# Performance work log

Hardware: AMD Instinct MI355X
Metric: run time of the kernel (lower is better)

Reference implementation:

```python
import jax, jax.numpy as jnp
import numpy as np

B, M, N, K = 8192, 512, 2048, 16
P = 50      # top-k support size per iteration
EPS = 0.01


def soft_threshold(x, theta, p):
    # x: [B, N]
    if p == 0:
        return jnp.sign(x) * jax.nn.relu(jnp.abs(x) - theta)
    abs_ = jnp.abs(x)
    topk_vals, _ = jax.lax.top_k(abs_, p)          # sorted descending
    thresh = topk_vals[:, -1]                      # min of top-k, per row
    keep = (abs_ > thresh[:, None]).astype(x.dtype)
    shrunk = jnp.sign(x) * jax.nn.relu(abs_ - theta)
    return keep * x + (1.0 - keep) * shrunk


def setup_inputs() -> dict:
    key = jax.random.key(0)
    k_y, k_A = jax.random.split(key)
    y = jax.random.normal(k_y, (B, M), dtype=jnp.float32)
    A = jax.random.normal(k_A, (M, N), dtype=jnp.float32) / np.sqrt(M)
    gamma = jnp.full((K,), 3.0, dtype=jnp.float32)
    theta = jnp.full((K,), 0.02, dtype=jnp.float32)
    a_param = jnp.full((K,), 0.01, dtype=jnp.float32)
    v = jnp.ones((K,), dtype=jnp.float32)
    vu = jnp.full((K,), 0.05, dtype=jnp.float32)
    theta_init = jnp.float32(1.0)
    return {"y": y, "A": A, "gamma": gamma, "theta": theta,
            "a_param": a_param, "v": v, "vu": vu,
            "theta_init": theta_init, "info": 0}


def reference(y, A, gamma, theta, a_param, v, vu, theta_init, info):
    # forward_op(x)  = x @ A.T   : [B,N] -> [B,M]
    # backward_op(b) = b @ A     : [B,M] -> [B,N]
    x = jnp.zeros((y.shape[0], A.shape[1]), dtype=y.dtype)
    for i in range(K):
        t = theta_init if i == 0 else theta[i]
        gain = 1.0 + t * vu[i] * jnp.exp(-v[i] * jnp.abs(x))
        b = (gain * x) @ A.T - y                 # residual in measurement space
        c = b @ A                                # gradient step direction
        x_new = soft_threshold(x - gamma[i] * c, theta[i], P)
        overshoot = 1.0 + a_param[i] / (jnp.abs(x_new - x) + EPS)
        x = overshoot * x_new + (1.0 - overshoot) * x
    return (x, jnp.zeros((K, 1), dtype=y.dtype), jnp.zeros((K, 1), dtype=y.dtype))
```

## Files before the change

### kernel.cpp

```cpp
#include <hip/hip_runtime.h>
#include <math.h>

#define Bsz  8192
#define Mdim 512
#define Ndim 2048
#define Kit  16
#define Pk   50
#define EPSv 0.01f

typedef __attribute__((ext_vector_type(8))) short bf16x8;
typedef __attribute__((ext_vector_type(4))) float f32x4;

static __device__ __forceinline__ unsigned short f2bf(float f) {
    unsigned u = __float_as_uint(f);
    return (unsigned short)((u + 0x7fffu + ((u >> 16) & 1u)) >> 16);
}
static __device__ __forceinline__ float bf2f(unsigned short h) {
    return __uint_as_float(((unsigned)h) << 16);
}

static __device__ __forceinline__ void gl16(const void* g, void* l) {
    __builtin_amdgcn_global_load_lds(
        (const __attribute__((address_space(1))) unsigned int*)g,
        (__attribute__((address_space(3))) unsigned int*)l, 16, 0, 0);
}

__global__ __launch_bounds__(256) void presplit_A(
    const float* __restrict__ A, unsigned short* __restrict__ Ah,
    unsigned short* __restrict__ Al, unsigned short* __restrict__ AhT,
    unsigned short* __restrict__ AlT)
{
    int idx = blockIdx.x * 256 + threadIdx.x;
    int m = idx >> 11, n = idx & (Ndim - 1);
    float a = A[idx];
    unsigned short h = f2bf(a);
    unsigned short l = f2bf(a - bf2f(h));
    Ah[idx] = h; Al[idx] = l;
    AhT[(size_t)n * Mdim + m] = h;
    AlT[(size_t)n * Mdim + m] = l;
}

__global__ __launch_bounds__(256) void split_negy_kernel(const float* __restrict__ y,
                                                         unsigned short* __restrict__ bS) {
    int i = blockIdx.x * 256 + threadIdx.x;
    float4 v = ((const float4*)y)[i];
    int idx = i * 4;
    int r = idx >> 9, c = idx & 511;
    float f0 = -v.x, f1 = -v.y, f2 = -v.z, f3 = -v.w;
    unsigned short h0 = f2bf(f0), h1 = f2bf(f1), h2 = f2bf(f2), h3 = f2bf(f3);
    ushort4 hv = make_ushort4(h0, h1, h2, h3);
    ushort4 lv = make_ushort4(f2bf(f0 - bf2f(h0)), f2bf(f1 - bf2f(h1)),
                              f2bf(f2 - bf2f(h2)), f2bf(f3 - bf2f(h3)));
    *(ushort4*)(bS + (size_t)r * 1024 + c)       = hv;
    *(ushort4*)(bS + (size_t)r * 1024 + 512 + c) = lv;
}

__global__ __launch_bounds__(256) void gemm1_mfma(
    const unsigned short* __restrict__ zS,
    const unsigned short* __restrict__ Ah, const unsigned short* __restrict__ Al,
    const float* __restrict__ y, unsigned short* __restrict__ bS)
{
    const int tid  = threadIdx.x;
    const int lane = tid & 63, w = tid >> 6;
    const int lm   = lane & 15, quad = lane >> 4;
    const int wr   = (w & 1) * 64, wm = (w >> 1) * 32;

    int d   = blockIdx.y * gridDim.x + blockIdx.x;
    int sid = (d & 7) * 64 + (d >> 3);
    const int m0 = (sid & 7) * 64, r0 = (sid >> 3) * 128;

    __shared__ __attribute__((aligned(16))) unsigned short zh_s[128 * 64];
    __shared__ __attribute__((aligned(16))) unsigned short zl_s[128 * 64];
    __shared__ __attribute__((aligned(16))) unsigned short ah_s[64 * 64];
    __shared__ __attribute__((aligned(16))) unsigned short al_s[64 * 64];

    f32x4 acc[4][2];
#pragma unroll
    for (int i = 0; i < 4; i++)
#pragma unroll
        for (int j = 0; j < 2; j++) acc[i][j] = (f32x4)0.f;

    const unsigned short* zsh[4]; const unsigned short* zsl[4]; int zoff[4];
#pragma unroll
    for (int s = 0; s < 4; s++) {
        int off = ((w * 4 + s) << 10) + lane * 16;
        int row = off >> 7;
        int kb  = (off & 127) ^ ((row & 7) << 4);
        zoff[s] = (w * 4 + s) << 10;
        zsh[s]  = zS + (size_t)(r0 + row) * 4096 + (kb >> 1);
        zsl[s]  = zS + (size_t)(r0 + row) * 4096 + 2048 + (kb >> 1);
    }
    const unsigned short* ash[2]; const unsigned short* asl[2]; int aoff[2];
#pragma unroll
    for (int s = 0; s < 2; s++) {
        int off = ((w * 2 + s) << 10) + lane * 16;
        int row = off >> 7;
        int kb  = (off & 127) ^ ((row & 7) << 4);
        aoff[s] = (w * 2 + s) << 10;
        ash[s]  = Ah + (size_t)(m0 + row) * 2048 + (kb >> 1);
        asl[s]  = Al + (size_t)(m0 + row) * 2048 + (kb >> 1);
    }

    const int X = (lm & 7) << 4;

    for (int k0 = 0; k0 < Ndim; k0 += 64) {
        __syncthreads();
#pragma unroll
        for (int s = 0; s < 4; s++) {
            gl16(zsh[s], (char*)zh_s + zoff[s]);
            gl16(zsl[s], (char*)zl_s + zoff[s]);
            zsh[s] += 64; zsl[s] += 64;
        }
#pragma unroll
        for (int s = 0; s < 2; s++) {
            gl16(ash[s], (char*)ah_s + aoff[s]);
            gl16(asl[s], (char*)al_s + aoff[s]);
            ash[s] += 64; asl[s] += 64;
        }
        __syncthreads();
#pragma unroll
        for (int kk = 0; kk < 2; kk++) {
            const int cbx = (kk * 64 + quad * 16) ^ X;
            bf16x8 bhf[2], blf[2];
#pragma unroll
            for (int fj = 0; fj < 2; fj++) {
                int ar = wm + fj * 16 + lm;
                bhf[fj] = *(const bf16x8*)((const char*)ah_s + ar * 128 + cbx);
                blf[fj] = *(const bf16x8*)((const char*)al_s + ar * 128 + cbx);
            }
#pragma unroll
            for (int fi = 0; fi < 4; fi++) {
                int zr = wr + fi * 16 + lm;
                bf16x8 zh8 = *(const bf16x8*)((const char*)zh_s + zr * 128 + cbx);
                bf16x8 zl8 = *(const bf16x8*)((const char*)zl_s + zr * 128 + cbx);
#pragma unroll
                for (int fj = 0; fj < 2; fj++) {
                    acc[fi][fj] = __builtin_amdgcn_mfma_f32_16x16x32_bf16(zh8, bhf[fj], acc[fi][fj], 0, 0, 0);
                    acc[fi][fj] = __builtin_amdgcn_mfma_f32_16x16x32_bf16(zh8, blf[fj], acc[fi][fj], 0, 0, 0);
                    acc[fi][fj] = __builtin_amdgcn_mfma_f32_16x16x32_bf16(zl8, bhf[fj], acc[fi][fj], 0, 0, 0);
                }
            }
        }
    }
#pragma unroll
    for (int fi = 0; fi < 4; fi++)
#pragma unroll
        for (int fj = 0; fj < 2; fj++)
#pragma unroll
            for (int r = 0; r < 4; r++) {
                int row = r0 + wr + fi * 16 + quad * 4 + r;
                int col = m0 + wm + fj * 16 + lm;
                float bv = acc[fi][fj][r] - y[(size_t)row * Mdim + col];
                unsigned short h = f2bf(bv);
                bS[(size_t)row * 1024 + col]       = h;
                bS[(size_t)row * 1024 + 512 + col] = f2bf(bv - bf2f(h));
            }
}

__global__ __launch_bounds__(256) void gemm2_mfma(
    const unsigned short* __restrict__ bS,
    const unsigned short* __restrict__ AhT, const unsigned short* __restrict__ AlT,
    float* __restrict__ c)
{
    const int tid  = threadIdx.x;
    const int lane = tid & 63, w = tid >> 6;
    const int lm   = lane & 15, quad = lane >> 4;
    const int wr   = (w & 1) * 64, wn = (w >> 1) * 64;

    int d   = blockIdx.y * gridDim.x + blockIdx.x;
    int sid = (d & 7) * 128 + (d >> 3);
    const int n0 = (sid & 15) * 128, r0 = (sid >> 4) * 128;

    __shared__ __attribute__((aligned(16))) unsigned short bh_s[128 * 32];
    __shared__ __attribute__((aligned(16))) unsigned short bl_s[128 * 32];
    __shared__ __attribute__((aligned(16))) unsigned short ath_s[128 * 32];
    __shared__ __attribute__((aligned(16))) unsigned short atl_s[128 * 32];

    f32x4 acc[4][4];
#pragma unroll
    for (int i = 0; i < 4; i++)
#pragma unroll
        for (int j = 0; j < 4; j++) acc[i][j] = (f32x4)0.f;

    const unsigned short *bsh[2], *bsl[2], *ash[2], *asl[2]; int coff[2];
#pragma unroll
    for (int s = 0; s < 2; s++) {
        int off = ((w * 2 + s) << 10) + lane * 16;
        int row = off >> 6;
        int kb  = (off & 63) ^ ((row & 3) << 4);
        coff[s] = (w * 2 + s) << 10;
        bsh[s]  = bS  + (size_t)(r0 + row) * 1024 + (kb >> 1);
        bsl[s]  = bS  + (size_t)(r0 + row) * 1024 + 512 + (kb >> 1);
        ash[s]  = AhT + (size_t)(n0 + row) * 512 + (kb >> 1);
        asl[s]  = AlT + (size_t)(n0 + row) * 512 + (kb >> 1);
    }

    const int X = (lm & 3) << 4;

    for (int k0 = 0; k0 < Mdim; k0 += 32) {
        __syncthreads();
#pragma unroll
        for (int s = 0; s < 2; s++) {
            gl16(bsh[s], (char*)bh_s + coff[s]);
            gl16(bsl[s], (char*)bl_s + coff[s]);
            gl16(ash[s], (char*)ath_s + coff[s]);
            gl16(asl[s], (char*)atl_s + coff[s]);
            bsh[s] += 32; bsl[s] += 32; ash[s] += 32; asl[s] += 32;
        }
        __syncthreads();
        const int cbx = (quad * 16) ^ X;
        bf16x8 ahf[4], alf[4];
#pragma unroll
        for (int fj = 0; fj < 4; fj++) {
            int ar = wn + fj * 16 + lm;
            ahf[fj] = *(const bf16x8*)((const char*)ath_s + ar * 64 + cbx);
            alf[fj] = *(const bf16x8*)((const char*)atl_s + ar * 64 + cbx);
        }
#pragma unroll
        for (int fi = 0; fi < 4; fi++) {
            int br = wr + fi * 16 + lm;
            bf16x8 bh8 = *(const bf16x8*)((const char*)bh_s + br * 64 + cbx);
            bf16x8 bl8 = *(const bf16x8*)((const char*)bl_s + br * 64 + cbx);
#pragma unroll
            for (int fj = 0; fj < 4; fj++) {
                acc[fi][fj] = __builtin_amdgcn_mfma_f32_16x16x32_bf16(bh8, ahf[fj], acc[fi][fj], 0, 0, 0);
                acc[fi][fj] = __builtin_amdgcn_mfma_f32_16x16x32_bf16(bh8, alf[fj], acc[fi][fj], 0, 0, 0);
                acc[fi][fj] = __builtin_amdgcn_mfma_f32_16x16x32_bf16(bl8, ahf[fj], acc[fi][fj], 0, 0, 0);
            }
        }
    }
#pragma unroll
    for (int fi = 0; fi < 4; fi++)
#pragma unroll
        for (int fj = 0; fj < 4; fj++)
#pragma unroll
            for (int r = 0; r < 4; r++) {
                int row = r0 + wr + fi * 16 + quad * 4 + r;
                int col = n0 + wn + fj * 16 + lm;
                c[(size_t)row * Ndim + col] = acc[fi][fj][r];
            }
}

__global__ __launch_bounds__(256) void topk_update_kernel(
    float* __restrict__ uz, float* __restrict__ x,
    const float* __restrict__ gamma, const float* __restrict__ theta,
    const float* __restrict__ a_param, const float* __restrict__ vv,
    const float* __restrict__ vu, int it)
{
    const int row = blockIdx.x;
    const int t   = threadIdx.x;
    float* crow = uz + (size_t)row * Ndim;
    float* xrow = x  + (size_t)row * Ndim;
    const float g = gamma[it];

    float4 c0 = *(const float4*)(crow + 4 * t);
    float4 c1 = *(const float4*)(crow + 4 * t + 1024);
    float4 x0 = *(const float4*)(xrow + 4 * t);
    float4 x1 = *(const float4*)(xrow + 4 * t + 1024);
    float cv[8] = { c0.x, c0.y, c0.z, c0.w, c1.x, c1.y, c1.z, c1.w };
    float xv[8] = { x0.x, x0.y, x0.z, x0.w, x1.x, x1.y, x1.z, x1.w };

    float uvals[8];
    unsigned keys[8];
#pragma unroll
    for (int e = 0; e < 8; e++) {
        uvals[e] = xv[e] - g * cv[e];
        keys[e]  = __float_as_uint(fabsf(uvals[e]));
    }

    __shared__ unsigned bins[256];
    __shared__ unsigned sel[2];

    unsigned prefix = 0;
    unsigned k = Pk;
#pragma unroll
    for (int pass = 0; pass < 4; ++pass) {
        const int shift = 24 - pass * 8;
        bins[t] = 0;
        __syncthreads();
        const unsigned himask = (pass == 0) ? 0u : (0xFFFFFFFFu << (shift + 8));
#pragma unroll
        for (int e = 0; e < 8; e++) {
            if ((keys[e] & himask) == prefix)
                atomicAdd(&bins[(keys[e] >> shift) & 255], 1u);
        }
        __syncthreads();
        if (t < 64) {
            const int i0 = 255 - 4 * t;
            unsigned c0b = bins[i0], c1b = bins[i0 - 1];
            unsigned c2b = bins[i0 - 2], c3b = bins[i0 - 3];
            unsigned s = c0b + c1b + c2b + c3b;
            unsigned sc = s;
#pragma unroll
            for (int off = 1; off < 64; off <<= 1) {
                unsigned o = __shfl_up(sc, (unsigned)off);
                if (t >= off) sc += o;
            }
            unsigned pre = sc - s;
            unsigned cs[4] = { c0b, c1b, c2b, c3b };
#pragma unroll
            for (int j = 0; j < 4; j++) {
                unsigned cb = cs[j];
                if (pre < k && pre + cb >= k) { sel[0] = (unsigned)(i0 - j); sel[1] = k - pre; }
                pre += cb;
            }
        }
        __syncthreads();
        prefix |= sel[0] << shift;
        k = sel[1];
    }
    const float thresh = __uint_as_float(prefix);

    const float th = theta[it];
    const float ap = a_param[it];
    const bool haveNext = (it + 1) < Kit;
    float tn = 0.f, vn = 0.f, vun = 0.f;
    if (haveNext) { tn = theta[it + 1]; vn = vv[it + 1]; vun = vu[it + 1]; }

    float xo[8];
    unsigned short zh8[8], zl8[8];
#pragma unroll
    for (int e = 0; e < 8; e++) {
        float uval = uvals[e];
        float au   = fabsf(uval);
        bool keep  = au > thresh;
        float shr  = copysignf(fmaxf(au - th, 0.f), uval);
        float xn   = keep ? uval : shr;
        float dlt  = xn - xv[e];
        float ov   = 1.f + ap / (fabsf(dlt) + EPSv);
        float xr   = xv[e] + ov * dlt;
        xo[e] = xr;
        float z = (1.f + tn * vun * __expf(-vn * fabsf(xr))) * xr;
        unsigned short h = f2bf(z);
        zh8[e] = h;
        zl8[e] = f2bf(z - bf2f(h));
    }
    float4 a0 = { xo[0], xo[1], xo[2], xo[3] };
    float4 a1 = { xo[4], xo[5], xo[6], xo[7] };
    *(float4*)(xrow + 4 * t) = a0;
    *(float4*)(xrow + 4 * t + 1024) = a1;
    if (haveNext) {
        unsigned short* zp = (unsigned short*)crow;
        *(ushort4*)(zp + 4 * t)        = make_ushort4(zh8[0], zh8[1], zh8[2], zh8[3]);
        *(ushort4*)(zp + 1024 + 4 * t) = make_ushort4(zh8[4], zh8[5], zh8[6], zh8[7]);
        *(ushort4*)(zp + 2048 + 4 * t) = make_ushort4(zl8[0], zl8[1], zl8[2], zl8[3]);
        *(ushort4*)(zp + 3072 + 4 * t) = make_ushort4(zl8[4], zl8[5], zl8[6], zl8[7]);
    }
}

extern "C" void kernel_launch(void* const* d_in, const int* in_sizes, int n_in,
                              void* d_out, int out_size, void* d_ws, size_t ws_size,
                              hipStream_t stream) {
    const float* y       = (const float*)d_in[0];
    const float* A       = (const float*)d_in[1];
    const float* gamma   = (const float*)d_in[2];
    const float* theta   = (const float*)d_in[3];
    const float* a_param = (const float*)d_in[4];
    const float* v       = (const float*)d_in[5];
    const float* vu      = (const float*)d_in[6];

    float* x = (float*)d_out;

    char* ws = (char*)d_ws;
    float*          uz = (float*)ws;
    unsigned short* bS = (unsigned short*)(ws + (size_t)Bsz * Ndim * 4);
    unsigned short* Ah = (unsigned short*)(ws + (size_t)80 * 1024 * 1024);
    unsigned short* Al  = Ah  + (size_t)Mdim * Ndim;
    unsigned short* AhT = Al  + (size_t)Mdim * Ndim;
    unsigned short* AlT = AhT + (size_t)Mdim * Ndim;

    hipMemsetAsync(d_out, 0, (size_t)out_size * sizeof(float), stream);

    dim3 blk(256);
    dim3 g1(Mdim / 64, Bsz / 128);
    dim3 g2(Ndim / 128, Bsz / 128);

    presplit_A<<<(Mdim * Ndim) / 256, blk, 0, stream>>>(A, Ah, Al, AhT, AlT);
    split_negy_kernel<<<(Bsz * Mdim / 4) / 256, blk, 0, stream>>>(y, bS);

    for (int it = 0; it < Kit; ++it) {
        if (it > 0)
            gemm1_mfma<<<g1, blk, 0, stream>>>((const unsigned short*)uz, Ah, Al, y, bS);
        gemm2_mfma<<<g2, blk, 0, stream>>>(bS, AhT, AlT, uz);
        topk_update_kernel<<<Bsz, blk, 0, stream>>>(uz, x, gamma, theta, a_param, v, vu, it);
    }
}
```

Before: 2.701 ms.

## Double-buffer LDS tiles in both MFMA GEMMs to overlap loads with compute

Measured after the change: 2.941 ms. 1.09x slower.

```diff
diff --git a/kernel.cpp b/kernel.cpp
--- a/kernel.cpp
+++ b/kernel.cpp
@@ -69,10 +69,10 @@
     int sid = (d & 7) * 64 + (d >> 3);
     const int m0 = (sid & 7) * 64, r0 = (sid >> 3) * 128;
 
-    __shared__ __attribute__((aligned(16))) unsigned short zh_s[128 * 64];
-    __shared__ __attribute__((aligned(16))) unsigned short zl_s[128 * 64];
-    __shared__ __attribute__((aligned(16))) unsigned short ah_s[64 * 64];
-    __shared__ __attribute__((aligned(16))) unsigned short al_s[64 * 64];
+    __shared__ __attribute__((aligned(16))) unsigned short zh_s[2][4096];
+    __shared__ __attribute__((aligned(16))) unsigned short zl_s[2][4096];
+    __shared__ __attribute__((aligned(16))) unsigned short ah_s[2][2048];
+    __shared__ __attribute__((aligned(16))) unsigned short al_s[2][2048];
 
     f32x4 acc[4][2];
 #pragma unroll
@@ -80,68 +80,81 @@
 #pragma unroll
         for (int j = 0; j < 2; j++) acc[i][j] = (f32x4)0.f;
 
-    const unsigned short* zsh[4]; const unsigned short* zsl[4]; int zoff[4];
-#pragma unroll
-    for (int s = 0; s < 4; s++) {
-        int off = ((w * 4 + s) << 10) + lane * 16;
-        int row = off >> 7;
-        int kb  = (off & 127) ^ ((row & 7) << 4);
-        zoff[s] = (w * 4 + s) << 10;
+    const unsigned short* zsh[2]; const unsigned short* zsl[2]; int zoff[2];
+#pragma unroll
+    for (int s = 0; s < 2; s++) {
+        int off = ((w * 2 + s) << 10) + lane * 16;
+        int row = off >> 6;
+        int kb  = (off & 63) ^ (((row >> 1) & 3) << 4);
+        zoff[s] = (w * 2 + s) << 10;
         zsh[s]  = zS + (size_t)(r0 + row) * 4096 + (kb >> 1);
         zsl[s]  = zS + (size_t)(r0 + row) * 4096 + 2048 + (kb >> 1);
     }
-    const unsigned short* ash[2]; const unsigned short* asl[2]; int aoff[2];
-#pragma unroll
-    for (int s = 0; s < 2; s++) {
-        int off = ((w * 2 + s) << 10) + lane * 16;
-        int row = off >> 7;
-        int kb  = (off & 127) ^ ((row & 7) << 4);
-        aoff[s] = (w * 2 + s) << 10;
-        ash[s]  = Ah + (size_t)(m0 + row) * 2048 + (kb >> 1);
-        asl[s]  = Al + (size_t)(m0 + row) * 2048 + (kb >> 1);
-    }
-
-    const int X = (lm & 7) << 4;
-
+    const unsigned short *ashp, *aslp; int aoff;
+    {
+        int off = (w << 10) + lane * 16;
+        int row = off >> 6;
+        int kb  = (off & 63) ^ (((row >> 1) & 3) << 4);
+        aoff = w << 10;
+        ashp = Ah + (size_t)(m0 + row) * 2048 + (kb >> 1);
+        aslp = Al + (size_t)(m0 + row) * 2048 + (kb >> 1);
+    }
+
+    const int X = ((lm >> 1) & 3) << 4;
+
+    auto STAGE = [&](int half) {
+        char* zhB = (char*)zh_s + half * 8192;
+        char* zlB = (char*)zl_s + half * 8192;
+        char* ahB = (char*)ah_s + half * 4096;
+        char* alB = (char*)al_s + half * 4096;
+#pragma unroll
+        for (int s = 0; s < 2; s++) {
+            gl16(zsh[s], zhB + zoff[s]);
+            gl16(zsl[s], zlB + zoff[s]);
+            zsh[s] += 32; zsl[s] += 32;
+        }
+        gl16(ashp, ahB + aoff);
+        gl16(aslp, alB + aoff);
+        ashp += 32; aslp += 32;
+    };
+
+    auto COMPUTE = [&](int half) {
+        const char* zhB = (const char*)zh_s + half * 8192;
+        const char* zlB = (const char*)zl_s + half * 8192;
+        const char* ahB = (const char*)ah_s + half * 4096;
+        const char* alB = (const char*)al_s + half * 4096;
+        const int cbx = (quad * 16) ^ X;
+        bf16x8 bhf[2], blf[2];
+#pragma unroll
+        for (int fj = 0; fj < 2; fj++) {
+            int ar = wm + fj * 16 + lm;
+            bhf[fj] = *(const bf16x8*)(ahB + ar * 64 + cbx);
+            blf[fj] = *(const bf16x8*)(alB + ar * 64 + cbx);
+        }
+#pragma unroll
+        for (int fi = 0; fi < 4; fi++) {
+            int zr = wr + fi * 16 + lm;
+            bf16x8 zh8 = *(const bf16x8*)(zhB + zr * 64 + cbx);
+            bf16x8 zl8 = *(const bf16x8*)(zlB + zr * 64 + cbx);
+#pragma unroll
+            for (int fj = 0; fj < 2; fj++) {
+                acc[fi][fj] = __builtin_amdgcn_mfma_f32_16x16x32_bf16(zh8, bhf[fj], acc[fi][fj], 0, 0, 0);
+                acc[fi][fj] = __builtin_amdgcn_mfma_f32_16x16x32_bf16(zh8, blf[fj], acc[fi][fj], 0, 0, 0);
+                acc[fi][fj] = __builtin_amdgcn_mfma_f32_16x16x32_bf16(zl8, bhf[fj], acc[fi][fj], 0, 0, 0);
+            }
+        }
+    };
+
+    STAGE(0);
     for (int k0 = 0; k0 < Ndim; k0 += 64) {
         __syncthreads();
-#pragma unroll
-        for (int s = 0; s < 4; s++) {
-            gl16(zsh[s], (char*)zh_s + zoff[s]);
-            gl16(zsl[s], (char*)zl_s + zoff[s]);
-            zsh[s] += 64; zsl[s] += 64;
-        }
-#pragma unroll
-        for (int s = 0; s < 2; s++) {
-            gl16(ash[s], (char*)ah_s + aoff[s]);
-            gl16(asl[s], (char*)al_s + aoff[s]);
-            ash[s] += 64; asl[s] += 64;
-        }
-        __syncthreads();
-#pragma unroll
-        for (int kk = 0; kk < 2; kk++) {
-            const int cbx = (kk * 64 + quad * 16) ^ X;
-            bf16x8 bhf[2], blf[2];
-#pragma unroll
-            for (int fj = 0; fj < 2; fj++) {
-                int ar = wm + fj * 16 + lm;
-                bhf[fj] = *(const bf16x8*)((const char*)ah_s + ar * 128 + cbx);
-                blf[fj] = *(const bf16x8*)((const char*)al_s + ar * 128 + cbx);
-            }
-#pragma unroll
-            for (int fi = 0; fi < 4; fi++) {
-                int zr = wr + fi * 16 + lm;
-                bf16x8 zh8 = *(const bf16x8*)((const char*)zh_s + zr * 128 + cbx);
-                bf16x8 zl8 = *(const bf16x8*)((const char*)zl_s + zr * 128 + cbx);
-#pragma unroll
-                for (int fj = 0; fj < 2; fj++) {
-                    acc[fi][fj] = __builtin_amdgcn_mfma_f32_16x16x32_bf16(zh8, bhf[fj], acc[fi][fj], 0, 0, 0);
-                    acc[fi][fj] = __builtin_amdgcn_mfma_f32_16x16x32_bf16(zh8, blf[fj], acc[fi][fj], 0, 0, 0);
-                    acc[fi][fj] = __builtin_amdgcn_mfma_f32_16x16x32_bf16(zl8, bhf[fj], acc[fi][fj], 0, 0, 0);
-                }
-            }
-        }
-    }
+        STAGE(1);
+        COMPUTE(0);
+        __syncthreads();
+        if (k0 + 64 < Ndim) STAGE(0);
+        COMPUTE(1);
+    }
+
 #pragma unroll
     for (int fi = 0; fi < 4; fi++)
 #pragma unroll
@@ -171,10 +184,10 @@
     int sid = (d & 7) * 128 + (d >> 3);
     const int n0 = (sid & 15) * 128, r0 = (sid >> 4) * 128;
 
-    __shared__ __attribute__((aligned(16))) unsigned short bh_s[128 * 32];
-    __shared__ __attribute__((aligned(16))) unsigned short bl_s[128 * 32];
-    __shared__ __attribute__((aligned(16))) unsigned short ath_s[128 * 32];
-    __shared__ __attribute__((aligned(16))) unsigned short atl_s[128 * 32];
+    __shared__ __attribute__((aligned(16))) unsigned short bh_s[2][4096];
+    __shared__ __attribute__((aligned(16))) unsigned short bl_s[2][4096];
+    __shared__ __attribute__((aligned(16))) unsigned short ath_s[2][4096];
+    __shared__ __attribute__((aligned(16))) unsigned short atl_s[2][4096];
 
     f32x4 acc[4][4];
 #pragma unroll
@@ -187,7 +200,7 @@
     for (int s = 0; s < 2; s++) {
         int off = ((w * 2 + s) << 10) + lane * 16;
         int row = off >> 6;
-        int kb  = (off & 63) ^ ((row & 3) << 4);
+        int kb  = (off & 63) ^ (((row >> 1) & 3) << 4);
         coff[s] = (w * 2 + s) << 10;
         bsh[s]  = bS  + (size_t)(r0 + row) * 1024 + (kb >> 1);
         bsl[s]  = bS  + (size_t)(r0 + row) * 1024 + 512 + (kb >> 1);
@@ -195,32 +208,41 @@
         asl[s]  = AlT + (size_t)(n0 + row) * 512 + (kb >> 1);
     }
 
-    const int X = (lm & 3) << 4;
-
-    for (int k0 = 0; k0 < Mdim; k0 += 32) {
-        __syncthreads();
+    const int X = ((lm >> 1) & 3) << 4;
+
+    auto STAGE = [&](int half) {
+        char* bhB = (char*)bh_s  + half * 8192;
+        char* blB = (char*)bl_s  + half * 8192;
+        char* ahB = (char*)ath_s + half * 8192;
+        char* alB = (char*)atl_s + half * 8192;
 #pragma unroll
         for (int s = 0; s < 2; s++) {
-            gl16(bsh[s], (char*)bh_s + coff[s]);
-            gl16(bsl[s], (char*)bl_s + coff[s]);
-            gl16(ash[s], (char*)ath_s + coff[s]);
-            gl16(asl[s], (char*)atl_s + coff[s]);
+            gl16(bsh[s], bhB + coff[s]);
+            gl16(bsl[s], blB + coff[s]);
+            gl16(ash[s], ahB + coff[s]);
+            gl16(asl[s], alB + coff[s]);
             bsh[s] += 32; bsl[s] += 32; ash[s] += 32; asl[s] += 32;
         }
-        __syncthreads();
+    };
+
+    auto COMPUTE = [&](int half) {
+        const char* bhB = (const char*)bh_s  + half * 8192;
+        const char* blB = (const char*)bl_s  + half * 8192;
+        const char* ahB = (const char*)ath_s + half * 8192;
+        const char* alB = (const char*)atl_s + half * 8192;
         const int cbx = (quad * 16) ^ X;
         bf16x8 ahf[4], alf[4];
 #pragma unroll
         for (int fj = 0; fj < 4; fj++) {
             int ar = wn + fj * 16 + lm;
-            ahf[fj] = *(const bf16x8*)((const char*)ath_s + ar * 64 + cbx);
-            alf[fj] = *(const bf16x8*)((const char*)atl_s + ar * 64 + cbx);
+            ahf[fj] = *(const bf16x8*)(ahB + ar * 64 + cbx);
+            alf[fj] = *(const bf16x8*)(alB + ar * 64 + cbx);
         }
 #pragma unroll
         for (int fi = 0; fi < 4; fi++) {
             int br = wr + fi * 16 + lm;
-            bf16x8 bh8 = *(const bf16x8*)((const char*)bh_s + br * 64 + cbx);
-            bf16x8 bl8 = *(const bf16x8*)((const char*)bl_s + br * 64 + cbx);
+            bf16x8 bh8 = *(const bf16x8*)(bhB + br * 64 + cbx);
+            bf16x8 bl8 = *(const bf16x8*)(blB + br * 64 + cbx);
 #pragma unroll
             for (int fj = 0; fj < 4; fj++) {
                 acc[fi][fj] = __builtin_amdgcn_mfma_f32_16x16x32_bf16(bh8, ahf[fj], acc[fi][fj], 0, 0, 0);
@@ -228,7 +250,18 @@
                 acc[fi][fj] = __builtin_amdgcn_mfma_f32_16x16x32_bf16(bl8, ahf[fj], acc[fi][fj], 0, 0, 0);
             }
         }
-    }
+    };
+
+    STAGE(0);
+    for (int k0 = 0; k0 < Mdim; k0 += 64) {
+        __syncthreads();
+        STAGE(1);
+        COMPUTE(0);
+        __syncthreads();
+        if (k0 + 64 < Mdim) STAGE(0);
+        COMPUTE(1);
+    }
+
 #pragma unroll
     for (int fi = 0; fi < 4; fi++)
 #pragma unroll
```

## Restructure gemm2 into 256x256 tiles with double-buffered LDS pipeline

Applied to the files above, without the earlier changes.

New measurement: 2.566 ms. -5.0%, faster.

```diff
diff --git a/kernel.cpp b/kernel.cpp
--- a/kernel.cpp
+++ b/kernel.cpp
@@ -24,6 +24,13 @@
         (const __attribute__((address_space(1))) unsigned int*)g,
         (__attribute__((address_space(3))) unsigned int*)l, 16, 0, 0);
 }
+
+#define PIPE_BARRIER() __builtin_amdgcn_s_barrier()
+
+#define MFMA3(acc_, bh_, bl_, ah_, al_)                                         \
+    acc_ = __builtin_amdgcn_mfma_f32_16x16x32_bf16(bh_, ah_, acc_, 0, 0, 0);    \
+    acc_ = __builtin_amdgcn_mfma_f32_16x16x32_bf16(bh_, al_, acc_, 0, 0, 0);    \
+    acc_ = __builtin_amdgcn_mfma_f32_16x16x32_bf16(bl_, ah_, acc_, 0, 0, 0);
 
 __global__ __launch_bounds__(256) void presplit_A(
     const float* __restrict__ A, unsigned short* __restrict__ Ah,
@@ -135,9 +142,7 @@
                 bf16x8 zl8 = *(const bf16x8*)((const char*)zl_s + zr * 128 + cbx);
 #pragma unroll
                 for (int fj = 0; fj < 2; fj++) {
-                    acc[fi][fj] = __builtin_amdgcn_mfma_f32_16x16x32_bf16(zh8, bhf[fj], acc[fi][fj], 0, 0, 0);
-                    acc[fi][fj] = __builtin_amdgcn_mfma_f32_16x16x32_bf16(zh8, blf[fj], acc[fi][fj], 0, 0, 0);
-                    acc[fi][fj] = __builtin_amdgcn_mfma_f32_16x16x32_bf16(zl8, bhf[fj], acc[fi][fj], 0, 0, 0);
+                    MFMA3(acc[fi][fj], zh8, zl8, bhf[fj], blf[fj]);
                 }
             }
         }
@@ -157,86 +162,124 @@
             }
 }
 
-__global__ __launch_bounds__(256) void gemm2_mfma(
+__global__ __launch_bounds__(512, 2) void gemm2_mfma(
     const unsigned short* __restrict__ bS,
     const unsigned short* __restrict__ AhT, const unsigned short* __restrict__ AlT,
     float* __restrict__ c)
 {
+    enum { NT = 16 };
     const int tid  = threadIdx.x;
     const int lane = tid & 63, w = tid >> 6;
     const int lm   = lane & 15, quad = lane >> 4;
-    const int wr   = (w & 1) * 64, wn = (w >> 1) * 64;
+    const int wrow = (w >> 2) * 128;
+    const int wcol = (w & 3) * 64;
 
     int d   = blockIdx.y * gridDim.x + blockIdx.x;
-    int sid = (d & 7) * 128 + (d >> 3);
-    const int n0 = (sid & 15) * 128, r0 = (sid >> 4) * 128;
-
-    __shared__ __attribute__((aligned(16))) unsigned short bh_s[128 * 32];
-    __shared__ __attribute__((aligned(16))) unsigned short bl_s[128 * 32];
-    __shared__ __attribute__((aligned(16))) unsigned short ath_s[128 * 32];
-    __shared__ __attribute__((aligned(16))) unsigned short atl_s[128 * 32];
-
-    f32x4 acc[4][4];
-#pragma unroll
-    for (int i = 0; i < 4; i++)
+    int sid = (d & 7) * 32 + (d >> 3);
+    const int n0 = (sid & 7) * 256, r0 = (sid >> 3) * 256;
+
+    __shared__ __attribute__((aligned(16))) unsigned short smem[2 * 32768];
+
+    f32x4 acc[8][4];
+#pragma unroll
+    for (int i = 0; i < 8; i++)
 #pragma unroll
         for (int j = 0; j < 4; j++) acc[i][j] = (f32x4)0.f;
 
-    const unsigned short *bsh[2], *bsl[2], *ash[2], *asl[2]; int coff[2];
+    const unsigned short *bhp[2], *blp[2], *ahp[2], *alp[2]; int doff[2];
 #pragma unroll
     for (int s = 0; s < 2; s++) {
         int off = ((w * 2 + s) << 10) + lane * 16;
         int row = off >> 6;
-        int kb  = (off & 63) ^ ((row & 3) << 4);
-        coff[s] = (w * 2 + s) << 10;
-        bsh[s]  = bS  + (size_t)(r0 + row) * 1024 + (kb >> 1);
-        bsl[s]  = bS  + (size_t)(r0 + row) * 1024 + 512 + (kb >> 1);
-        ash[s]  = AhT + (size_t)(n0 + row) * 512 + (kb >> 1);
-        asl[s]  = AlT + (size_t)(n0 + row) * 512 + (kb >> 1);
-    }
-
-    const int X = (lm & 3) << 4;
-
-    for (int k0 = 0; k0 < Mdim; k0 += 32) {
-        __syncthreads();
+        int kb  = (off & 63) ^ (((row >> 1) & 3) << 4);
+        doff[s] = (w * 2 + s) << 10;
+        bhp[s]  = bS  + (size_t)(r0 + row) * 1024 + (kb >> 1);
+        blp[s]  = bS  + (size_t)(r0 + row) * 1024 + 512 + (kb >> 1);
+        ahp[s]  = AhT + (size_t)(n0 + row) * 512 + (kb >> 1);
+        alp[s]  = AlT + (size_t)(n0 + row) * 512 + (kb >> 1);
+    }
+
+    const int X   = ((lm >> 1) & 3) << 4;
+    const int cbx = (quad * 16) ^ X;
+
+    auto STAGE = [&](int t) {
+        char* base = (char*)smem + (t & 1) * 65536;
+        const int ko = t * 32;
 #pragma unroll
         for (int s = 0; s < 2; s++) {
-            gl16(bsh[s], (char*)bh_s + coff[s]);
-            gl16(bsl[s], (char*)bl_s + coff[s]);
-            gl16(ash[s], (char*)ath_s + coff[s]);
-            gl16(asl[s], (char*)atl_s + coff[s]);
-            bsh[s] += 32; bsl[s] += 32; ash[s] += 32; asl[s] += 32;
-        }
-        __syncthreads();
-        const int cbx = (quad * 16) ^ X;
-        bf16x8 ahf[4], alf[4];
+            gl16(bhp[s] + ko, base +     0 + doff[s]);
+            gl16(blp[s] + ko, base + 16384 + doff[s]);
+            gl16(ahp[s] + ko, base + 32768 + doff[s]);
+            gl16(alp[s] + ko, base + 49152 + doff[s]);
+        }
+    };
+
+    STAGE(0);
+    asm volatile("s_waitcnt vmcnt(0)" ::: "memory");
+    PIPE_BARRIER();
+
+#pragma unroll 2
+    for (int t = 0; t < NT; ++t) {
+        const char* B0  = (const char*)smem + (t & 1) * 65536;
+        const char* bhB = B0, *blB = B0 + 16384;
+        const char* ahB = B0 + 32768, *alB = B0 + 49152;
+
+        bf16x8 ahf[4], alf[4], bhf[4], blf[4];
 #pragma unroll
         for (int fj = 0; fj < 4; fj++) {
-            int ar = wn + fj * 16 + lm;
-            ahf[fj] = *(const bf16x8*)((const char*)ath_s + ar * 64 + cbx);
-            alf[fj] = *(const bf16x8*)((const char*)atl_s + ar * 64 + cbx);
+            int ar = wcol + fj * 16 + lm;
+            ahf[fj] = *(const bf16x8*)(ahB + ar * 64 + cbx);
+            alf[fj] = *(const bf16x8*)(alB + ar * 64 + cbx);
         }
 #pragma unroll
         for (int fi = 0; fi < 4; fi++) {
-            int br = wr + fi * 16 + lm;
-            bf16x8 bh8 = *(const bf16x8*)((const char*)bh_s + br * 64 + cbx);
-            bf16x8 bl8 = *(const bf16x8*)((const char*)bl_s + br * 64 + cbx);
+            int br = wrow + fi * 16 + lm;
+            bhf[fi] = *(const bf16x8*)(bhB + br * 64 + cbx);
+            blf[fi] = *(const bf16x8*)(blB + br * 64 + cbx);
+        }
+        if (t + 1 < NT) STAGE(t + 1);
+        PIPE_BARRIER();
+        asm volatile("s_waitcnt lgkmcnt(0)" ::: "memory");
+        __builtin_amdgcn_sched_barrier(0);
+        __builtin_amdgcn_s_setprio(1);
+#pragma unroll
+        for (int fi = 0; fi < 4; fi++)
 #pragma unroll
             for (int fj = 0; fj < 4; fj++) {
-                acc[fi][fj] = __builtin_amdgcn_mfma_f32_16x16x32_bf16(bh8, ahf[fj], acc[fi][fj], 0, 0, 0);
-                acc[fi][fj] = __builtin_amdgcn_mfma_f32_16x16x32_bf16(bh8, alf[fj], acc[fi][fj], 0, 0, 0);
-                acc[fi][fj] = __builtin_amdgcn_mfma_f32_16x16x32_bf16(bl8, ahf[fj], acc[fi][fj], 0, 0, 0);
-            }
-        }
-    }
-#pragma unroll
-    for (int fi = 0; fi < 4; fi++)
+                MFMA3(acc[fi][fj], bhf[fi], blf[fi], ahf[fj], alf[fj]);
+            }
+        __builtin_amdgcn_s_setprio(0);
+        PIPE_BARRIER();
+
+#pragma unroll
+        for (int fi = 0; fi < 4; fi++) {
+            int br = wrow + (fi + 4) * 16 + lm;
+            bhf[fi] = *(const bf16x8*)(bhB + br * 64 + cbx);
+            blf[fi] = *(const bf16x8*)(blB + br * 64 + cbx);
+        }
+        PIPE_BARRIER();
+        asm volatile("s_waitcnt lgkmcnt(0)" ::: "memory");
+        __builtin_amdgcn_sched_barrier(0);
+        __builtin_amdgcn_s_setprio(1);
+#pragma unroll
+        for (int fi = 0; fi < 4; fi++)
+#pragma unroll
+            for (int fj = 0; fj < 4; fj++) {
+                MFMA3(acc[fi + 4][fj], bhf[fi], blf[fi], ahf[fj], alf[fj]);
+            }
+        __builtin_amdgcn_s_setprio(0);
+        asm volatile("s_waitcnt vmcnt(0)" ::: "memory");
+        PIPE_BARRIER();
+    }
+
+#pragma unroll
+    for (int fi = 0; fi < 8; fi++)
 #pragma unroll
         for (int fj = 0; fj < 4; fj++)
 #pragma unroll
             for (int r = 0; r < 4; r++) {
-                int row = r0 + wr + fi * 16 + quad * 4 + r;
-                int col = n0 + wn + fj * 16 + lm;
+                int row = r0 + wrow + fi * 16 + quad * 4 + r;
+                int col = n0 + wcol + fj * 16 + lm;
                 c[(size_t)row * Ndim + col] = acc[fi][fj][r];
             }
 }
@@ -371,17 +414,16 @@
 
     hipMemsetAsync(d_out, 0, (size_t)out_size * sizeof(float), stream);
 
-    dim3 blk(256);
     dim3 g1(Mdim / 64, Bsz / 128);
-    dim3 g2(Ndim / 128, Bsz / 128);
-
-    presplit_A<<<(Mdim * Ndim) / 256, blk, 0, stream>>>(A, Ah, Al, AhT, AlT);
-    split_negy_kernel<<<(Bsz * Mdim / 4) / 256, blk, 0, stream>>>(y, bS);
+    dim3 g2(Ndim / 256, Bsz / 256);
+
+    presplit_A<<<(Mdim * Ndim) / 256, dim3(256), 0, stream>>>(A, Ah, Al, AhT, AlT);
+    split_negy_kernel<<<(Bsz * Mdim / 4) / 256, dim3(256), 0, stream>>>(y, bS);
 
     for (int it = 0; it < Kit; ++it) {
         if (it > 0)
-            gemm1_mfma<<<g1, blk, 0, stream>>>((const unsigned short*)uz, Ah, Al, y, bS);
-        gemm2_mfma<<<g2, blk, 0, stream>>>(bS, AhT, AlT, uz);
-        topk_update_kernel<<<Bsz, blk, 0, stream>>>(uz, x, gamma, theta, a_param, v, vu, it);
-    }
-}
+            gemm1_mfma<<<g1, dim3(256), 0, stream>>>((const unsigned short*)uz, Ah, Al, y, bS);
+        gemm2_mfma<<<g2, dim3(512), 0, stream>>>(bS, AhT, AlT, uz);
+        topk_update_kernel<<<Bsz, dim3(256), 0, stream>>>(uz, x, gamma, theta, a_param, v, vu, it);
+    }
+}
```
